# Performance work log

Hardware: AMD Instinct MI355X
Metric: run time of the kernel (lower is better)

Reference implementation:

```python
import jax, jax.numpy as jnp
import numpy as np

B, P, H, D = 32, 512, 512, 512

def setup_inputs() -> dict:
    key = jax.random.key(0)
    k1, k2, k3, k4 = jax.random.split(key, 4)
    px = jax.random.normal(k1, (B, P, D), dtype=jnp.float32)
    hx = jax.random.normal(k2, (B, H, D), dtype=jnp.float32)
    p_mask = jax.random.randint(k3, (B, P), 0, 2) == 1  # True = padded
    h_mask = jax.random.randint(k4, (B, H), 0, 2) == 1
    return {"px": px, "hx": hx, "p_mask": p_mask, "h_mask": h_mask}

def reference(px, hx, p_mask, h_mask):
    # shared (unscaled) score matrix: [B, P, H]
    e = jnp.einsum('bpd,bhd->bph', px, hx)
    neg_inf = jnp.float32(-jnp.inf)
    h_bias = jnp.where(h_mask, neg_inf, 0.0).astype(e.dtype)  # [B, H]
    p_bias = jnp.where(p_mask, neg_inf, 0.0).astype(e.dtype)  # [B, P]
    # softmax over hypothesis axis -> attend px to hx
    weight_b = jax.nn.softmax(e + h_bias[:, None, :], axis=2)  # [B, P, H]
    px_hat = jnp.einsum('bph,bhd->bpd', weight_b, hx)
    # softmax over premise axis -> attend hx to px
    weight_a = jax.nn.softmax(e + p_bias[:, :, None], axis=1)  # [B, P, H]
    hx_hat = jnp.einsum('bph,bpd->bhd', weight_a, px)
    m_p = jnp.concatenate([px, px_hat, px - px_hat, px * px_hat], axis=-1)
    m_h = jnp.concatenate([hx, hx_hat, hx - hx_hat, hx * hx_hat], axis=-1)
    return (m_p, m_h)
```

## Files before the change

### kernel.cpp

```cpp
#include <hip/hip_runtime.h>
#include <math.h>

#define NB 32
#define NN 512
#define ROWC 2048ull

typedef __attribute__((ext_vector_type(8))) short bf16x8;
typedef __attribute__((ext_vector_type(4))) float f32x4;

__device__ __forceinline__ unsigned int fbits(float f) {
  union { float f; unsigned int u; } v; v.f = f; return v.u;
}
__device__ __forceinline__ float bcast(unsigned int u) {
  union { unsigned int u; float f; } v; v.u = u; return v.f;
}
__device__ __forceinline__ unsigned int bf16_rne(float f) {
  unsigned int b = fbits(f);
  return (b + 0x7FFFu + ((b >> 16) & 1u)) >> 16;
}

__device__ __forceinline__ int frag_byte(int blk, int lane, int khalf) {
  int base = ((((khalf << 3) + blk) << 6) + lane) << 4;
  int swz = (blk ^ (lane >> 4) ^ (khalf << 2)) & 7;
  return base ^ (swz << 4);
}

__device__ __forceinline__ int frag32(int blk, int lane) {
  int base = (blk << 10) + (lane << 4);
  int swz = (blk ^ (lane >> 4)) & 7;
  return base ^ (swz << 4);
}

__global__ __launch_bounds__(256) void gemm_e(
    const float* __restrict__ px, const float* __restrict__ hx,
    float* __restrict__ e) {
  __shared__ union {
    struct { char Ah[8192]; char Al[8192]; char Bh[8192]; char Bl[8192]; } s;
    float ep[64][132];
  } u;
  const int b = blockIdx.z;
  const float* A = px + (size_t)b * NN * NN;
  const float* B = hx + (size_t)b * NN * NN;
  float* C = e + (size_t)b * NN * NN;
  const int row0 = blockIdx.y * 128, col0 = blockIdx.x * 128;
  const int t = threadIdx.x;
  const int l = t & 63, w = t >> 6;
  const int wr = w >> 1, wc = w & 1;

  f32x4 acc[4][4];
#pragma unroll
  for (int i = 0; i < 4; ++i)
#pragma unroll
    for (int j = 0; j < 4; ++j)
#pragma unroll
      for (int r = 0; r < 4; ++r) acc[i][j][r] = 0.f;

  for (int k0 = 0; k0 < NN; k0 += 32) {
#pragma unroll
    for (int i = 0; i < 4; ++i) {
      int idx = i * 256 + t;
      int r = idx >> 3, c4 = idx & 7, k = c4 << 2;
      int byte = frag32(r >> 4, (r & 15) + ((c4 >> 1) << 4)) + (c4 & 1) * 8;
      float4 f = *(const float4*)&A[(size_t)(row0 + r) * NN + k0 + k];
      unsigned int b0 = fbits(f.x), b1 = fbits(f.y), b2 = fbits(f.z), b3 = fbits(f.w);
      unsigned int h01 = (b0 >> 16) | (b1 & 0xFFFF0000u);
      unsigned int h23 = (b2 >> 16) | (b3 & 0xFFFF0000u);
      float r0 = f.x - bcast(b0 & 0xFFFF0000u);
      float r1 = f.y - bcast(b1 & 0xFFFF0000u);
      float r2 = f.z - bcast(b2 & 0xFFFF0000u);
      float r3 = f.w - bcast(b3 & 0xFFFF0000u);
      unsigned int l01 = (fbits(r0) >> 16) | (fbits(r1) & 0xFFFF0000u);
      unsigned int l23 = (fbits(r2) >> 16) | (fbits(r3) & 0xFFFF0000u);
      *(uint2*)&u.s.Ah[byte] = make_uint2(h01, h23);
      *(uint2*)&u.s.Al[byte] = make_uint2(l01, l23);
    }
#pragma unroll
    for (int i = 0; i < 4; ++i) {
      int idx = i * 256 + t;
      int r = idx >> 3, c4 = idx & 7, k = c4 << 2;
      int byte = frag32(r >> 4, (r & 15) + ((c4 >> 1) << 4)) + (c4 & 1) * 8;
      float4 f = *(const float4*)&B[(size_t)(col0 + r) * NN + k0 + k];
      unsigned int b0 = fbits(f.x), b1 = fbits(f.y), b2 = fbits(f.z), b3 = fbits(f.w);
      unsigned int h01 = (b0 >> 16) | (b1 & 0xFFFF0000u);
      unsigned int h23 = (b2 >> 16) | (b3 & 0xFFFF0000u);
      float r0 = f.x - bcast(b0 & 0xFFFF0000u);
      float r1 = f.y - bcast(b1 & 0xFFFF0000u);
      float r2 = f.z - bcast(b2 & 0xFFFF0000u);
      float r3 = f.w - bcast(b3 & 0xFFFF0000u);
      unsigned int l01 = (fbits(r0) >> 16) | (fbits(r1) & 0xFFFF0000u);
      unsigned int l23 = (fbits(r2) >> 16) | (fbits(r3) & 0xFFFF0000u);
      *(uint2*)&u.s.Bh[byte] = make_uint2(h01, h23);
      *(uint2*)&u.s.Bl[byte] = make_uint2(l01, l23);
    }
    __syncthreads();

    bf16x8 ah[4], al[4];
#pragma unroll
    for (int i = 0; i < 4; ++i) {
      int ab = frag32(wr * 4 + i, l);
      ah[i] = *(const bf16x8*)&u.s.Ah[ab];
      al[i] = *(const bf16x8*)&u.s.Al[ab];
    }
#pragma unroll
    for (int j = 0; j < 4; ++j) {
      int bb = frag32(wc * 4 + j, l);
      bf16x8 bh = *(const bf16x8*)&u.s.Bh[bb];
      bf16x8 bl = *(const bf16x8*)&u.s.Bl[bb];
#pragma unroll
      for (int i = 0; i < 4; ++i) {
        acc[i][j] = __builtin_amdgcn_mfma_f32_16x16x32_bf16(al[i], bh, acc[i][j], 0, 0, 0);
        acc[i][j] = __builtin_amdgcn_mfma_f32_16x16x32_bf16(ah[i], bl, acc[i][j], 0, 0, 0);
        acc[i][j] = __builtin_amdgcn_mfma_f32_16x16x32_bf16(ah[i], bh, acc[i][j], 0, 0, 0);
      }
    }
    __syncthreads();
  }

  const int g = l >> 4, li = l & 15;
#pragma unroll
  for (int pass = 0; pass < 2; ++pass) {
    if (wr == pass) {
#pragma unroll
      for (int i = 0; i < 4; ++i)
#pragma unroll
        for (int j = 0; j < 4; ++j)
#pragma unroll
          for (int r = 0; r < 4; ++r)
            u.ep[i * 16 + g * 4 + r][wc * 64 + j * 16 + li] = acc[i][j][r];
    }
    __syncthreads();
#pragma unroll
    for (int i = 0; i < 8; ++i) {
      int idx = i * 256 + t;
      int r = idx >> 5, c4 = idx & 31;
      int grow = row0 + pass * 64 + r;
      float4 v = *(const float4*)&u.ep[r][c4 * 4];
      *(float4*)&C[(size_t)grow * NN + col0 + c4 * 4] = v;
    }
    __syncthreads();
  }
}

__global__ __launch_bounds__(512) void row_stats(
    const float* __restrict__ e, const int* __restrict__ h_mask,
    float* __restrict__ rmax, float* __restrict__ rinv) {
  const int b = blockIdx.x, oct = blockIdx.y;
  __shared__ int hm[512];
  const int t = threadIdx.x;
  if (t < 128) *(int4*)&hm[t * 4] = *(const int4*)&h_mask[(size_t)b * NN + t * 4];
  __syncthreads();
  const int row = oct * 64 + (t >> 3), seg = t & 7;
  const float* er = e + (size_t)b * NN * NN + (size_t)row * NN + seg * 64;
  float m = -INFINITY, s = 0.f;
#pragma unroll
  for (int i = 0; i < 16; ++i) {
    float4 f = *(const float4*)&er[i * 4];
    int4 msk = *(const int4*)&hm[seg * 64 + i * 4];
    float vv[4] = {f.x, f.y, f.z, f.w};
    int mk[4] = {msk.x, msk.y, msk.z, msk.w};
#pragma unroll
    for (int c = 0; c < 4; ++c) {
      if (!mk[c]) {
        float mn = fmaxf(m, vv[c]);
        s = s * __expf(m - mn) + __expf(vv[c] - mn);
        m = mn;
      }
    }
  }
#pragma unroll
  for (int o = 1; o < 8; o <<= 1) {
    float m2 = __shfl_xor(m, o), s2 = __shfl_xor(s, o);
    float mn = fmaxf(m, m2);
    float sn = 0.f;
    if (s > 0.f) sn += s * __expf(m - mn);
    if (s2 > 0.f) sn += s2 * __expf(m2 - mn);
    m = mn; s = sn;
  }
  if (seg == 0) {
    rmax[(size_t)b * NN + row] = m;
    rinv[(size_t)b * NN + row] = 1.0f / s;
  }
}

__global__ __launch_bounds__(512) void col_stats(
    const float* __restrict__ e, const int* __restrict__ p_mask,
    float* __restrict__ cmax, float* __restrict__ cinv) {
  const int b = blockIdx.x, oct = blockIdx.y;
  __shared__ int pm[512];
  const int t = threadIdx.x;
  if (t < 128) *(int4*)&pm[t * 4] = *(const int4*)&p_mask[(size_t)b * NN + t * 4];
  __syncthreads();
  const int col = oct * 64 + (t >> 3), seg = t & 7;
  const float* ec = e + (size_t)b * NN * NN + col;
  float m = -INFINITY, s = 0.f;
#pragma unroll 8
  for (int i = 0; i < 64; ++i) {
    int p = seg * 64 + i;
    if (!pm[p]) {
      float v = ec[(size_t)p * NN];
      float mn = fmaxf(m, v);
      s = s * __expf(m - mn) + __expf(v - mn);
      m = mn;
    }
  }
#pragma unroll
  for (int o = 1; o < 8; o <<= 1) {
    float m2 = __shfl_xor(m, o), s2 = __shfl_xor(s, o);
    float mn = fmaxf(m, m2);
    float sn = 0.f;
    if (s > 0.f) sn += s * __expf(m - mn);
    if (s2 > 0.f) sn += s2 * __expf(m2 - mn);
    m = mn; s = sn;
  }
  if (seg == 0) {
    cmax[(size_t)b * NN + col] = m;
    cinv[(size_t)b * NN + col] = 1.0f / s;
  }
}

__global__ __launch_bounds__(256) void gemm_wp(
    const float* __restrict__ E, const float* __restrict__ hxg,
    const float* __restrict__ pxg, const int* __restrict__ h_mask,
    const float* __restrict__ rmax, const float* __restrict__ rinv,
    float* __restrict__ outg) {
  __shared__ union {
    struct { char A[16384]; char B[16384]; } s;
    float ep[64][132];
  } u;
  const int b = blockIdx.z;
  const float* Eb = E + (size_t)b * NN * NN;
  const float* B = hxg + (size_t)b * NN * NN;
  const float* X = pxg + (size_t)b * NN * NN;
  const int* hm = h_mask + (size_t)b * NN;
  const float* rmx = rmax + (size_t)b * NN;
  const float* rin = rinv + (size_t)b * NN;
  float* out = outg + (size_t)b * NN * ROWC;
  const int row0 = blockIdx.y * 128, col0 = blockIdx.x * 128;
  const int t = threadIdx.x;
  const int l = t & 63, w = t >> 6;
  const int wr = w >> 1, wc = w & 1;

  float rmv[8];
#pragma unroll
  for (int i = 0; i < 8; ++i) rmv[i] = rmx[row0 + ((i * 256 + t) >> 4)];

  f32x4 acc[4][4];
#pragma unroll
  for (int i = 0; i < 4; ++i)
#pragma unroll
    for (int j = 0; j < 4; ++j)
#pragma unroll
      for (int r = 0; r < 4; ++r) acc[i][j][r] = 0.f;

  for (int k0 = 0; k0 < NN; k0 += 64) {
#pragma unroll
    for (int i = 0; i < 8; ++i) {
      int idx = i * 256 + t;
      int r = idx >> 4, c4 = idx & 15, k = c4 << 2;
      float4 f = *(const float4*)&Eb[(size_t)(row0 + r) * NN + k0 + k];
      int4 m4 = *(const int4*)&hm[k0 + k];
      float w0 = m4.x ? 0.f : __expf(f.x - rmv[i]);
      float w1 = m4.y ? 0.f : __expf(f.y - rmv[i]);
      float w2 = m4.z ? 0.f : __expf(f.z - rmv[i]);
      float w3 = m4.w ? 0.f : __expf(f.w - rmv[i]);
      unsigned int p01 = bf16_rne(w0) | (bf16_rne(w1) << 16);
      unsigned int p23 = bf16_rne(w2) | (bf16_rne(w3) << 16);
      int khalf = k >> 5, k8 = (k >> 3) & 3, j = k & 7;
      int byte = frag_byte(r >> 4, (r & 15) + (k8 << 4), khalf) + (j << 1);
      *(uint2*)&u.s.A[byte] = make_uint2(p01, p23);
    }
#pragma unroll
    for (int i = 0; i < 4; ++i) {
      int idx = i * 256 + t;
      int kp = idx >> 5, nq = idx & 31;
      int k = kp << 1, n = nq << 2;
      const float* p0 = &B[(size_t)(k0 + k) * NN + col0 + n];
      float4 f0 = *(const float4*)p0;
      float4 f1 = *(const float4*)(p0 + NN);
      int khalf = k >> 5, k8 = (k >> 3) & 3, j = k & 7;
      float fa0[4] = {f0.x, f0.y, f0.z, f0.w};
      float fa1[4] = {f1.x, f1.y, f1.z, f1.w};
#pragma unroll
      for (int c = 0; c < 4; ++c) {
        unsigned int pk = bf16_rne(fa0[c]) | (bf16_rne(fa1[c]) << 16);
        int nn2 = n + c;
        int byte = frag_byte(nn2 >> 4, (nn2 & 15) + (k8 << 4), khalf) + (j << 1);
        *(unsigned int*)&u.s.B[byte] = pk;
      }
    }
    __syncthreads();
#pragma unroll
    for (int kh = 0; kh < 2; ++kh) {
      bf16x8 av[4], bv[4];
#pragma unroll
      for (int i = 0; i < 4; ++i) {
        av[i] = *(const bf16x8*)&u.s.A[frag_byte(wr * 4 + i, l, kh)];
        bv[i] = *(const bf16x8*)&u.s.B[frag_byte(wc * 4 + i, l, kh)];
      }
#pragma unroll
      for (int i = 0; i < 4; ++i)
#pragma unroll
        for (int j = 0; j < 4; ++j)
          acc[i][j] = __builtin_amdgcn_mfma_f32_16x16x32_bf16(av[i], bv[j], acc[i][j], 0, 0, 0);
    }
    __syncthreads();
  }

  const int g = l >> 4, li = l & 15;
#pragma unroll
  for (int pass = 0; pass < 2; ++pass) {
    if (wr == pass) {
#pragma unroll
      for (int i = 0; i < 4; ++i)
#pragma unroll
        for (int j = 0; j < 4; ++j)
#pragma unroll
          for (int r = 0; r < 4; ++r)
            u.ep[i * 16 + g * 4 + r][wc * 64 + j * 16 + li] = acc[i][j][r];
    }
    __syncthreads();
#pragma unroll
    for (int i = 0; i < 8; ++i) {
      int idx = i * 256 + t;
      int r = idx >> 5, c4 = idx & 31;
      int grow = row0 + pass * 64 + r;
      float ri = rin[grow];
      float4 ph = *(const float4*)&u.ep[r][c4 * 4];
      ph.x *= ri; ph.y *= ri; ph.z *= ri; ph.w *= ri;
      float4 xv = *(const float4*)&X[(size_t)grow * NN + col0 + c4 * 4];
      size_t base = (size_t)grow * ROWC + col0 + c4 * 4;
      *(float4*)&out[base] = xv;
      *(float4*)&out[base + 512] = ph;
      float4 df = {xv.x - ph.x, xv.y - ph.y, xv.z - ph.z, xv.w - ph.w};
      *(float4*)&out[base + 1024] = df;
      float4 pr = {xv.x * ph.x, xv.y * ph.y, xv.z * ph.z, xv.w * ph.w};
      *(float4*)&out[base + 1536] = pr;
    }
    __syncthreads();
  }
}

__global__ __launch_bounds__(256) void gemm_wh(
    const float* __restrict__ E, const float* __restrict__ pxg,
    const float* __restrict__ hxg, const int* __restrict__ p_mask,
    const float* __restrict__ cmax, const float* __restrict__ cinv,
    float* __restrict__ outg) {
  __shared__ union {
    struct { char A[16384]; char B[16384]; } s;
    float ep[64][132];
  } u;
  const int b = blockIdx.z;
  const float* Eb = E + (size_t)b * NN * NN;
  const float* B = pxg + (size_t)b * NN * NN;
  const float* X = hxg + (size_t)b * NN * NN;
  const int* pmsk = p_mask + (size_t)b * NN;
  const float* cmx = cmax + (size_t)b * NN;
  const float* cin = cinv + (size_t)b * NN;
  float* out = outg + (size_t)b * NN * ROWC;
  const int row0 = blockIdx.y * 128, col0 = blockIdx.x * 128;
  const int t = threadIdx.x;
  const int l = t & 63, w = t >> 6;
  const int wr = w >> 1, wc = w & 1;

  float4 cmv[4];
#pragma unroll
  for (int i = 0; i < 4; ++i) {
    int idx = i * 256 + t;
    int n = (idx & 31) << 2;
    cmv[i] = *(const float4*)&cmx[row0 + n];
  }

  f32x4 acc[4][4];
#pragma unroll
  for (int i = 0; i < 4; ++i)
#pragma unroll
    for (int j = 0; j < 4; ++j)
#pragma unroll
      for (int r = 0; r < 4; ++r) acc[i][j][r] = 0.f;

  for (int k0 = 0; k0 < NN; k0 += 64) {
#pragma unroll
    for (int i = 0; i < 4; ++i) {
      int idx = i * 256 + t;
      int kp = idx >> 5, nq = idx & 31;
      int k = kp << 1, n = nq << 2;
      const float* p0 = &Eb[(size_t)(k0 + k) * NN + row0 + n];
      float4 f0 = *(const float4*)p0;
      float4 f1 = *(const float4*)(p0 + NN);
      int pm0 = pmsk[k0 + k], pm1 = pmsk[k0 + k + 1];
      float fa0[4] = {f0.x, f0.y, f0.z, f0.w};
      float fa1[4] = {f1.x, f1.y, f1.z, f1.w};
      float cma[4] = {cmv[i].x, cmv[i].y, cmv[i].z, cmv[i].w};
      int khalf = k >> 5, k8 = (k >> 3) & 3, j = k & 7;
#pragma unroll
      for (int c = 0; c < 4; ++c) {
        float w0 = pm0 ? 0.f : __expf(fa0[c] - cma[c]);
        float w1 = pm1 ? 0.f : __expf(fa1[c] - cma[c]);
        unsigned int pk = bf16_rne(w0) | (bf16_rne(w1) << 16);
        int nn2 = n + c;
        int byte = frag_byte(nn2 >> 4, (nn2 & 15) + (k8 << 4), khalf) + (j << 1);
        *(unsigned int*)&u.s.A[byte] = pk;
      }
    }
#pragma unroll
    for (int i = 0; i < 4; ++i) {
      int idx = i * 256 + t;
      int kp = idx >> 5, nq = idx & 31;
      int k = kp << 1, n = nq << 2;
      const float* p0 = &B[(size_t)(k0 + k) * NN + col0 + n];
      float4 f0 = *(const float4*)p0;
      float4 f1 = *(const float4*)(p0 + NN);
      int khalf = k >> 5, k8 = (k >> 3) & 3, j = k & 7;
      float fa0[4] = {f0.x, f0.y, f0.z, f0.w};
      float fa1[4] = {f1.x, f1.y, f1.z, f1.w};
#pragma unroll
      for (int c = 0; c < 4; ++c) {
        unsigned int pk = bf16_rne(fa0[c]) | (bf16_rne(fa1[c]) << 16);
        int nn2 = n + c;
        int byte = frag_byte(nn2 >> 4, (nn2 & 15) + (k8 << 4), khalf) + (j << 1);
        *(unsigned int*)&u.s.B[byte] = pk;
      }
    }
    __syncthreads();
#pragma unroll
    for (int kh = 0; kh < 2; ++kh) {
      bf16x8 av[4], bv[4];
#pragma unroll
      for (int i = 0; i < 4; ++i) {
        av[i] = *(const bf16x8*)&u.s.A[frag_byte(wr * 4 + i, l, kh)];
        bv[i] = *(const bf16x8*)&u.s.B[frag_byte(wc * 4 + i, l, kh)];
      }
#pragma unroll
      for (int i = 0; i < 4; ++i)
#pragma unroll
        for (int j = 0; j < 4; ++j)
          acc[i][j] = __builtin_amdgcn_mfma_f32_16x16x32_bf16(av[i], bv[j], acc[i][j], 0, 0, 0);
    }
    __syncthreads();
  }

  const int g = l >> 4, li = l & 15;
#pragma unroll
  for (int pass = 0; pass < 2; ++pass) {
    if (wr == pass) {
#pragma unroll
      for (int i = 0; i < 4; ++i)
#pragma unroll
        for (int j = 0; j < 4; ++j)
#pragma unroll
          for (int r = 0; r < 4; ++r)
            u.ep[i * 16 + g * 4 + r][wc * 64 + j * 16 + li] = acc[i][j][r];
    }
    __syncthreads();
#pragma unroll
    for (int i = 0; i < 8; ++i) {
      int idx = i * 256 + t;
      int r = idx >> 5, c4 = idx & 31;
      int grow = row0 + pass * 64 + r;
      float ci = cin[grow];
      float4 hh = *(const float4*)&u.ep[r][c4 * 4];
      hh.x *= ci; hh.y *= ci; hh.z *= ci; hh.w *= ci;
      float4 xv = *(const float4*)&X[(size_t)grow * NN + col0 + c4 * 4];
      size_t base = (size_t)grow * ROWC + col0 + c4 * 4;
      *(float4*)&out[base] = xv;
      *(float4*)&out[base + 512] = hh;
      float4 df = {xv.x - hh.x, xv.y - hh.y, xv.z - hh.z, xv.w - hh.w};
      *(float4*)&out[base + 1024] = df;
      float4 pr = {xv.x * hh.x, xv.y * hh.y, xv.z * hh.z, xv.w * hh.w};
      *(float4*)&out[base + 1536] = pr;
    }
    __syncthreads();
  }
}

extern "C" void kernel_launch(void* const* d_in, const int* in_sizes, int n_in,
                              void* d_out, int out_size, void* d_ws, size_t ws_size,
                              hipStream_t stream) {
  const float* px = (const float*)d_in[0];
  const float* hx = (const float*)d_in[1];
  const int* p_mask = (const int*)d_in[2];
  const int* h_mask = (const int*)d_in[3];
  float* out = (float*)d_out;

  float* E = (float*)d_ws;
  float* rmaxv = E + (size_t)NB * NN * NN;
  float* rinvv = rmaxv + (size_t)NB * NN;
  float* cmaxv = rinvv + (size_t)NB * NN;
  float* cinvv = cmaxv + (size_t)NB * NN;

  dim3 gg(4, 4, NB);
  gemm_e<<<gg, dim3(256), 0, stream>>>(px, hx, E);
  row_stats<<<dim3(NB, 8), dim3(512), 0, stream>>>(E, h_mask, rmaxv, rinvv);
  col_stats<<<dim3(NB, 8), dim3(512), 0, stream>>>(E, p_mask, cmaxv, cinvv);
  gemm_wp<<<gg, dim3(256), 0, stream>>>(E, hx, px, h_mask, rmaxv, rinvv, out);
  gemm_wh<<<gg, dim3(256), 0, stream>>>(E, px, hx, p_mask, cmaxv, cinvv,
                                        out + (size_t)NB * NN * ROWC);
}
```

Baseline: 247.0 us.

## Load MFMA fragments directly from global memory, dropping LDS staging in gemm_e

The score GEMM no longer stages bf16 hi/lo splits of px and hx tiles through shared memory with swizzled layouts and barriers. Each wave now loads its own fp32 fragments straight from global memory into registers, splits them into hi/lo bf16, and feeds the MFMAs, removing LDS traffic and __syncthreads from the k-loop. The cost is redundant global/L2 reads, since the two waves sharing a row or column tile each load and convert the same data, and the 32-byte-per-lane strided accesses are less coalesced. The MFMA issue order is also regrouped into three loops per j.

```diff
diff --git a/kernel.cpp b/kernel.cpp
--- a/kernel.cpp
+++ b/kernel.cpp
@@ -17,6 +17,18 @@
 __device__ __forceinline__ unsigned int bf16_rne(float f) {
   unsigned int b = fbits(f);
   return (b + 0x7FFFu + ((b >> 16) & 1u)) >> 16;
+}
+
+__device__ __forceinline__ void frag_hilo(float4 f0, float4 f1,
+                                          bf16x8& hi, bf16x8& lo) {
+  float f[8] = {f0.x, f0.y, f0.z, f0.w, f1.x, f1.y, f1.z, f1.w};
+#pragma unroll
+  for (int q = 0; q < 8; ++q) {
+    unsigned int bq = fbits(f[q]);
+    hi[q] = (short)(bq >> 16);
+    float r = f[q] - bcast(bq & 0xFFFF0000u);
+    lo[q] = (short)(fbits(r) >> 16);
+  }
 }
 
 __device__ __forceinline__ int frag_byte(int blk, int lane, int khalf) {
@@ -25,19 +37,10 @@
   return base ^ (swz << 4);
 }
 
-__device__ __forceinline__ int frag32(int blk, int lane) {
-  int base = (blk << 10) + (lane << 4);
-  int swz = (blk ^ (lane >> 4)) & 7;
-  return base ^ (swz << 4);
-}
-
 __global__ __launch_bounds__(256) void gemm_e(
     const float* __restrict__ px, const float* __restrict__ hx,
     float* __restrict__ e) {
-  __shared__ union {
-    struct { char Ah[8192]; char Al[8192]; char Bh[8192]; char Bl[8192]; } s;
-    float ep[64][132];
-  } u;
+  __shared__ float ep[64][132];
   const int b = blockIdx.z;
   const float* A = px + (size_t)b * NN * NN;
   const float* B = hx + (size_t)b * NN * NN;
@@ -46,6 +49,7 @@
   const int t = threadIdx.x;
   const int l = t & 63, w = t >> 6;
   const int wr = w >> 1, wc = w & 1;
+  const int fr = l & 15, fk = (l >> 4) * 8;
 
   f32x4 acc[4][4];
 #pragma unroll
@@ -55,65 +59,39 @@
 #pragma unroll
       for (int r = 0; r < 4; ++r) acc[i][j][r] = 0.f;
 
+  const float* pa[4];
+  const float* pb[4];
+#pragma unroll
+  for (int i = 0; i < 4; ++i)
+    pa[i] = A + (size_t)(row0 + wr * 64 + i * 16 + fr) * NN + fk;
+#pragma unroll
+  for (int j = 0; j < 4; ++j)
+    pb[j] = B + (size_t)(col0 + wc * 64 + j * 16 + fr) * NN + fk;
+
   for (int k0 = 0; k0 < NN; k0 += 32) {
+    bf16x8 ah[4], al[4];
 #pragma unroll
     for (int i = 0; i < 4; ++i) {
-      int idx = i * 256 + t;
-      int r = idx >> 3, c4 = idx & 7, k = c4 << 2;
-      int byte = frag32(r >> 4, (r & 15) + ((c4 >> 1) << 4)) + (c4 & 1) * 8;
-      float4 f = *(const float4*)&A[(size_t)(row0 + r) * NN + k0 + k];
-      unsigned int b0 = fbits(f.x), b1 = fbits(f.y), b2 = fbits(f.z), b3 = fbits(f.w);
-      unsigned int h01 = (b0 >> 16) | (b1 & 0xFFFF0000u);
-      unsigned int h23 = (b2 >> 16) | (b3 & 0xFFFF0000u);
-      float r0 = f.x - bcast(b0 & 0xFFFF0000u);
-      float r1 = f.y - bcast(b1 & 0xFFFF0000u);
-      float r2 = f.z - bcast(b2 & 0xFFFF0000u);
-      float r3 = f.w - bcast(b3 & 0xFFFF0000u);
-      unsigned int l01 = (fbits(r0) >> 16) | (fbits(r1) & 0xFFFF0000u);
-      unsigned int l23 = (fbits(r2) >> 16) | (fbits(r3) & 0xFFFF0000u);
-      *(uint2*)&u.s.Ah[byte] = make_uint2(h01, h23);
-      *(uint2*)&u.s.Al[byte] = make_uint2(l01, l23);
-    }
-#pragma unroll
-    for (int i = 0; i < 4; ++i) {
-      int idx = i * 256 + t;
-      int r = idx >> 3, c4 = idx & 7, k = c4 << 2;
-      int byte = frag32(r >> 4, (r & 15) + ((c4 >> 1) << 4)) + (c4 & 1) * 8;
-      float4 f = *(const float4*)&B[(size_t)(col0 + r) * NN + k0 + k];
-      unsigned int b0 = fbits(f.x), b1 = fbits(f.y), b2 = fbits(f.z), b3 = fbits(f.w);
-      unsigned int h01 = (b0 >> 16) | (b1 & 0xFFFF0000u);
-      unsigned int h23 = (b2 >> 16) | (b3 & 0xFFFF0000u);
-      float r0 = f.x - bcast(b0 & 0xFFFF0000u);
-      float r1 = f.y - bcast(b1 & 0xFFFF0000u);
-      float r2 = f.z - bcast(b2 & 0xFFFF0000u);
-      float r3 = f.w - bcast(b3 & 0xFFFF0000u);
-      unsigned int l01 = (fbits(r0) >> 16) | (fbits(r1) & 0xFFFF0000u);
-      unsigned int l23 = (fbits(r2) >> 16) | (fbits(r3) & 0xFFFF0000u);
-      *(uint2*)&u.s.Bh[byte] = make_uint2(h01, h23);
-      *(uint2*)&u.s.Bl[byte] = make_uint2(l01, l23);
-    }
-    __syncthreads();
-
-    bf16x8 ah[4], al[4];
-#pragma unroll
-    for (int i = 0; i < 4; ++i) {
-      int ab = frag32(wr * 4 + i, l);
-      ah[i] = *(const bf16x8*)&u.s.Ah[ab];
-      al[i] = *(const bf16x8*)&u.s.Al[ab];
+      float4 f0 = *(const float4*)(pa[i] + k0);
+      float4 f1 = *(const float4*)(pa[i] + k0 + 4);
+      frag_hilo(f0, f1, ah[i], al[i]);
     }
 #pragma unroll
     for (int j = 0; j < 4; ++j) {
-      int bb = frag32(wc * 4 + j, l);
-      bf16x8 bh = *(const bf16x8*)&u.s.Bh[bb];
-      bf16x8 bl = *(const bf16x8*)&u.s.Bl[bb];
-#pragma unroll
-      for (int i = 0; i < 4; ++i) {
+      float4 g0 = *(const float4*)(pb[j] + k0);
+      float4 g1 = *(const float4*)(pb[j] + k0 + 4);
+      bf16x8 bh, bl;
+      frag_hilo(g0, g1, bh, bl);
+#pragma unroll
+      for (int i = 0; i < 4; ++i)
         acc[i][j] = __builtin_amdgcn_mfma_f32_16x16x32_bf16(al[i], bh, acc[i][j], 0, 0, 0);
+#pragma unroll
+      for (int i = 0; i < 4; ++i)
         acc[i][j] = __builtin_amdgcn_mfma_f32_16x16x32_bf16(ah[i], bl, acc[i][j], 0, 0, 0);
+#pragma unroll
+      for (int i = 0; i < 4; ++i)
         acc[i][j] = __builtin_amdgcn_mfma_f32_16x16x32_bf16(ah[i], bh, acc[i][j], 0, 0, 0);
-      }
-    }
-    __syncthreads();
+    }
   }
 
   const int g = l >> 4, li = l & 15;
@@ -126,7 +104,7 @@
         for (int j = 0; j < 4; ++j)
 #pragma unroll
           for (int r = 0; r < 4; ++r)
-            u.ep[i * 16 + g * 4 + r][wc * 64 + j * 16 + li] = acc[i][j][r];
+            ep[i * 16 + g * 4 + r][wc * 64 + j * 16 + li] = acc[i][j][r];
     }
     __syncthreads();
 #pragma unroll
@@ -134,7 +112,7 @@
       int idx = i * 256 + t;
       int r = idx >> 5, c4 = idx & 31;
       int grow = row0 + pass * 64 + r;
-      float4 v = *(const float4*)&u.ep[r][c4 * 4];
+      float4 v = *(const float4*)&ep[r][c4 * 4];
       *(float4*)&C[(size_t)grow * NN + col0 + c4 * 4] = v;
     }
     __syncthreads();
```

After: 232.8 us. 5.8% less time.
